# Kernel optimization log

Hardware: AMD Instinct MI355X
Metric: run time of the kernel (lower is better)

The kernel has to match this reference:

```python
import jax, jax.numpy as jnp
import numpy as np

DIM = 1536
N_HEADS = 12
HEAD_DIM = DIM // N_HEADS  # 128
EPS = 1e-6
B, L = 2, 2048


def _rms_norm(x, g, eps=EPS):
    # WanRMSNorm: normalize in fp32 over last dim, scale by g
    xf = x.astype(jnp.float32)
    y = xf * jax.lax.rsqrt(jnp.mean(xf * xf, axis=-1, keepdims=True) + eps)
    return (y * g).astype(x.dtype)


def _apply_rotary(x, freqs):
    # x: [b, s, n, d]; freqs: [1, s, 2d] -> cos/sin each [1, s, 1, d]
    cos, sin = jnp.split(freqs[:, :, None, :], 2, axis=-1)
    b, s, n, d = x.shape
    xr = x.reshape(b, s, n, d // 2, 2)
    rot = jnp.stack([-xr[..., 1], xr[..., 0]], axis=-1).reshape(b, s, n, d)
    out = x.astype(jnp.float32) * cos + rot.astype(jnp.float32) * sin
    return out.astype(x.dtype)


def setup_inputs() -> dict:
    key = jax.random.key(0)
    ks = jax.random.split(key, 12)
    scale = 1.0 / np.sqrt(DIM)
    x = jax.random.normal(ks[0], (B, L, DIM), dtype=jnp.float32)
    wq = jax.random.normal(ks[1], (DIM, DIM), dtype=jnp.float32) * scale
    bq = jnp.zeros((DIM,), dtype=jnp.float32)
    wk = jax.random.normal(ks[2], (DIM, DIM), dtype=jnp.float32) * scale
    bk = jnp.zeros((DIM,), dtype=jnp.float32)
    wv = jax.random.normal(ks[3], (DIM, DIM), dtype=jnp.float32) * scale
    bv = jnp.zeros((DIM,), dtype=jnp.float32)
    wo = jax.random.normal(ks[4], (DIM, DIM), dtype=jnp.float32) * scale
    bo = jnp.zeros((DIM,), dtype=jnp.float32)
    gq = jnp.ones((DIM,), dtype=jnp.float32)
    gk = jnp.ones((DIM,), dtype=jnp.float32)
    # real RoPE table: interleaved-pair cos/sin, concatenated -> [1, L, 2*HEAD_DIM]
    half = HEAD_DIM // 2
    inv_freq = 1.0 / (10000.0 ** (np.arange(half, dtype=np.float32) / half))
    ang = np.arange(L, dtype=np.float32)[:, None] * inv_freq[None, :]  # [L, half]
    cos = np.repeat(np.cos(ang), 2, axis=-1)  # [L, HEAD_DIM]
    sin = np.repeat(np.sin(ang), 2, axis=-1)
    freqs = jnp.asarray(np.concatenate([cos, sin], axis=-1)[None])  # [1, L, 2*HEAD_DIM]
    seq_lens = jnp.array([L, 3 * L // 4], dtype=jnp.int32)
    grid_sizes = jnp.array([[16, 16, 8], [16, 12, 8]], dtype=jnp.int32)
    return {"x": x, "wq": wq, "bq": bq, "wk": wk, "bk": bk, "wv": wv, "bv": bv,
            "wo": wo, "bo": bo, "gq": gq, "gk": gk, "freqs": freqs,
            "seq_lens": seq_lens, "grid_sizes": grid_sizes}


def reference(x, wq, bq, wk, bk, wv, bv, wo, bo, gq, gk, freqs, seq_lens, grid_sizes):
    b, s, _ = x.shape
    n, d = N_HEADS, HEAD_DIM
    q = _rms_norm(x @ wq.T + bq, gq).reshape(b, s, n, d)
    k = _rms_norm(x @ wk.T + bk, gk).reshape(b, s, n, d)
    v = (x @ wv.T + bv).reshape(b, s, n, d)
    q = _apply_rotary(q, freqs)
    k = _apply_rotary(k, freqs)
    # variable-length attention: mask keys j >= seq_lens[b]; window (-1,-1) = full
    scores = jnp.einsum("bqnd,bknd->bnqk", q, k) * (1.0 / np.sqrt(d))
    key_mask = (jnp.arange(s)[None, :] < seq_lens[:, None])[:, None, None, :]  # [b,1,1,s]
    scores = jnp.where(key_mask, scores, jnp.finfo(scores.dtype).min)
    probs = jax.nn.softmax(scores, axis=-1)
    out = jnp.einsum("bnqk,bknd->bqnd", probs, v).reshape(b, s, n * d)
    return out @ wo.T + bo
```

## Files before the change

### kernel.cpp

```cpp
#include <hip/hip_runtime.h>
#include <stdint.h>

typedef unsigned short u16;
typedef __bf16 bfx8 __attribute__((ext_vector_type(8)));
typedef short  sx4  __attribute__((ext_vector_type(4)));
typedef float  fx4  __attribute__((ext_vector_type(4)));
typedef float  fx16 __attribute__((ext_vector_type(16)));
typedef u16    ux8  __attribute__((ext_vector_type(8)));
typedef u16    ux4  __attribute__((ext_vector_type(4)));
typedef float  flt4 __attribute__((ext_vector_type(4)));

#define DIM   1536
#define NH    12
#define HD    128
#define BATCH 2
#define SEQ   2048
#define MTOK  (BATCH*SEQ)
#define EPSV  1e-6f
#define SCALE 0.08838834764831845f
#define NX    (MTOK*DIM)
#define NW    (DIM*DIM)

__device__ __forceinline__ u16 f2bf(float x){
  union { float f; uint32_t u; } v; v.f = x;
  return (u16)((v.u + 0x7FFFu + ((v.u >> 16) & 1u)) >> 16);
}
__device__ __forceinline__ float bf2f(u16 h){
  union { uint32_t u; float f; } v; v.u = ((uint32_t)h) << 16; return v.f;
}
__device__ __forceinline__ void gl_lds16(const void* g, void* l){
  __builtin_amdgcn_global_load_lds((const __attribute__((address_space(1))) void*)g,
                                   (__attribute__((address_space(3))) void*)l, 16, 0, 0);
}
__device__ __forceinline__ fx4 fzero(){ fx4 z = {0.f,0.f,0.f,0.f}; return z; }

__global__ __launch_bounds__(256)
void convert_k(const float* __restrict__ x, const float* __restrict__ wq,
               const float* __restrict__ wk, const float* __restrict__ wv,
               const float* __restrict__ wo,
               u16* __restrict__ xb, u16* __restrict__ wqb, u16* __restrict__ wkb,
               u16* __restrict__ wvb, u16* __restrict__ wob)
{
  const long i4 = (long)(blockIdx.x * 256 + threadIdx.x) * 4;
  const float* src; u16* dst; long off;
  if (i4 < NX){ src = x; dst = xb; off = i4; }
  else {
    long j = i4 - NX;
    if      (j < (long)NW)   { src = wq; dst = wqb; off = j; }
    else if (j < 2L*NW)      { src = wk; dst = wkb; off = j - NW; }
    else if (j < 3L*NW)      { src = wv; dst = wvb; off = j - 2L*NW; }
    else                     { src = wo; dst = wob; off = j - 3L*NW; }
  }
  flt4 v = *(const flt4*)(src + off);
  ux4 o;
  o[0] = f2bf(v[0]); o[1] = f2bf(v[1]); o[2] = f2bf(v[2]); o[3] = f2bf(v[3]);
  *(ux4*)(dst + off) = o;
}

#define BM 128
#define BN 128
#define BK 64
#define NKIT (DIM/BK)

template<int MODE>
__device__ __forceinline__ void gemm_core(char* smem,
                                          const u16* __restrict__ A, const u16* __restrict__ W,
                                          const float* __restrict__ bias,
                                          u16* __restrict__ outb, float* __restrict__ outf,
                                          float* __restrict__ sumsq, u16* __restrict__ vtout)
{
  const int t = threadIdx.x;
  const int lane = t & 63;
  const int wid = t >> 6;
  const int wm = wid >> 1, wn = wid & 1;
  const int quad = lane >> 4, l15 = lane & 15;

  const int lin = blockIdx.y * 12 + blockIdx.x;
  const int r   = lin >> 3;
  const int m0  = ((lin & 7) + 8 * (r / 12)) * BM;
  const int n0  = (r % 12) * BN;

  fx4 acc[4][4];
  #pragma unroll
  for (int i = 0; i < 4; ++i)
    #pragma unroll
    for (int j = 0; j < 4; ++j) acc[i][j] = fzero();

  const int ri  = t >> 3;
  const int sg0 = t & 7;

  auto stage = [&](int kb, int p){
    const int k0 = kb * BK;
    char* base = smem + p * 32768;
    #pragma unroll
    for (int s = 0; s < 4; ++s){
      const int row = s*32 + ri;
      const int sa = sg0 ^ (row & 7);
      gl_lds16(A + (size_t)(m0+row)*DIM + k0 + sa*8, base + s*4096 + t*16);
      gl_lds16(W + (size_t)(n0+row)*DIM + k0 + sa*8, base + 16384 + s*4096 + t*16);
    }
  };

  stage(0, 0);
  for (int kb = 0; kb < NKIT; ++kb){
    char* cur = smem + (kb & 1) * 32768;
    __syncthreads();
    if (kb + 1 < NKIT) stage(kb + 1, (kb + 1) & 1);
    #pragma unroll
    for (int kk = 0; kk < 2; ++kk){
      bfx8 af[4], bw[4];
      #pragma unroll
      for (int i = 0; i < 4; ++i){
        const int rA = wm*64 + i*16 + l15;
        af[i] = *(const bfx8*)(cur + rA*128 + (((kk*4 + quad) ^ (rA & 7)) * 16));
        const int rB = wn*64 + i*16 + l15;
        bw[i] = *(const bfx8*)(cur + 16384 + rB*128 + (((kk*4 + quad) ^ (rB & 7)) * 16));
      }
      #pragma unroll
      for (int i = 0; i < 4; ++i)
        #pragma unroll
        for (int j = 0; j < 4; ++j)
          acc[i][j] = __builtin_amdgcn_mfma_f32_16x16x32_bf16(af[i], bw[j], acc[i][j], 0, 0, 0);
    }
  }

  float bvals[4];
  #pragma unroll
  for (int j = 0; j < 4; ++j) bvals[j] = bias[n0 + wn*64 + j*16 + l15];

  if (MODE == 1){
    u16* T = (u16*)smem;
    #pragma unroll
    for (int i = 0; i < 4; ++i){
      const int row0  = wm*64 + i*16 + quad*4;
      const int chunk = row0 >> 3;
      const int half  = quad & 1;
      #pragma unroll
      for (int j = 0; j < 4; ++j){
        const int col = wn*64 + j*16 + l15;
        ux4 w4;
        #pragma unroll
        for (int rr = 0; rr < 4; ++rr) w4[rr] = f2bf(acc[i][j][rr] + bvals[j]);
        *(ux4*)((char*)T + col*256 + ((chunk ^ (col & 15)) << 4) + half*8) = w4;
      }
    }
    __syncthreads();
    const int b   = m0 >> 11;
    const int m0l = m0 & (SEQ - 1);
    const int cr  = t & 15;
    #pragma unroll
    for (int s = 0; s < 8; ++s){
      const int cl = s*16 + (t >> 4);
      const ux8 v = *(const ux8*)((char*)T + cl*256 + ((cr ^ (cl & 15)) << 4));
      const int cg = n0 + cl;
      const int hh = cg >> 7, dd = cg & (HD - 1);
      *(ux8*)(vtout + (size_t)((b*NH + hh)*HD + dd)*SEQ + m0l + cr*8) = v;
    }
    return;
  }

  #pragma unroll
  for (int i = 0; i < 4; ++i){
    #pragma unroll
    for (int rr = 0; rr < 4; ++rr){
      const int grow = m0 + wm*64 + i*16 + quad*4 + rr;
      float s2 = 0.f;
      #pragma unroll
      for (int j = 0; j < 4; ++j){
        const int gcol = n0 + wn*64 + j*16 + l15;
        const float v = acc[i][j][rr] + bvals[j];
        if (MODE == 2) outf[(size_t)grow*DIM + gcol] = v;
        else           outb[(size_t)grow*DIM + gcol] = f2bf(v);
        s2 += v*v;
      }
      if (MODE == 0){
        s2 += __shfl_xor(s2, 1);
        s2 += __shfl_xor(s2, 2);
        s2 += __shfl_xor(s2, 4);
        s2 += __shfl_xor(s2, 8);
        if (l15 == 0) atomicAdd(&sumsq[grow], s2);
      }
    }
  }
}

__global__ __launch_bounds__(256)
void gemm_qkv_k(const u16* __restrict__ xb,
                const u16* __restrict__ wqb, const u16* __restrict__ wkb, const u16* __restrict__ wvb,
                const float* __restrict__ bq, const float* __restrict__ bk, const float* __restrict__ bv,
                u16* __restrict__ qraw, u16* __restrict__ kraw, u16* __restrict__ vt,
                float* __restrict__ ssq, float* __restrict__ ssk)
{
  __shared__ char smem[65536];
  const int z = blockIdx.z;
  if (z == 0)      gemm_core<0>(smem, xb, wqb, bq, qraw, nullptr, ssq, nullptr);
  else if (z == 1) gemm_core<0>(smem, xb, wkb, bk, kraw, nullptr, ssk, nullptr);
  else             gemm_core<1>(smem, xb, wvb, bv, nullptr, nullptr, nullptr, vt);
}

__global__ __launch_bounds__(256)
void gemm_out_k(const u16* __restrict__ attnb, const u16* __restrict__ wob,
                const float* __restrict__ bo, float* __restrict__ out)
{
  __shared__ char smem[65536];
  gemm_core<2>(smem, attnb, wob, bo, nullptr, out, nullptr, nullptr);
}

__global__ __launch_bounds__(256)
void normrope_k(const u16* __restrict__ qraw, const u16* __restrict__ kraw,
                const float* __restrict__ ssq, const float* __restrict__ ssk,
                const float* __restrict__ gq, const float* __restrict__ gk,
                const float* __restrict__ freqs,
                u16* __restrict__ qbf, u16* __restrict__ kbf)
{
  const int row = blockIdx.x;
  const int isK = blockIdx.y;
  const u16* src   = isK ? kraw : qraw;
  const float* ss  = isK ? ssk  : ssq;
  const float* g   = isK ? gk   : gq;
  u16* dst         = isK ? kbf  : qbf;
  const int spos = row & (SEQ - 1);
  float rstd = rsqrtf(ss[row] * (1.0f/DIM) + EPSV);
  if (!isK) rstd *= SCALE;
  #pragma unroll
  for (int it = 0; it < 3; ++it){
    const int p = threadIdx.x + it*256;
    const int d = p*2;
    const int hd = d & (HD-1);
    const uint32_t two = *(const uint32_t*)(src + (size_t)row*DIM + d);
    const float y0 = bf2f((u16)(two & 0xFFFFu)) * rstd * g[d];
    const float y1 = bf2f((u16)(two >> 16))     * rstd * g[d+1];
    const float c  = freqs[spos*(2*HD) + hd];
    const float sn = freqs[spos*(2*HD) + HD + hd];
    const float o0 = y0*c - y1*sn;
    const float o1 = y1*c + y0*sn;
    *(uint32_t*)(dst + (size_t)row*DIM + d) = (uint32_t)f2bf(o0) | ((uint32_t)f2bf(o1) << 16);
  }
}

__global__ __launch_bounds__(256, 3)
void flash_k(const u16* __restrict__ qbf, const u16* __restrict__ kbf, const u16* __restrict__ vt,
             const int* __restrict__ seq_lens, u16* __restrict__ attnb)
{
  __shared__ char smem[50176];
  const int t = threadIdx.x;
  const int lane = t & 63;
  const int h = lane >> 5;
  const int l31 = lane & 31;
  const int wq = (t >> 6) & 1;
  const int wk = t >> 7;

  const int u  = blockIdx.x;
  const int qt = (u >> 3) & 31;
  const int pr = (u & 7) + 8 * (u >> 8);
  const int hh = pr % 12;
  const int b  = pr / 12;

  const int q0 = qt * 64 + wq * 32;
  const int tokbase = b * SEQ;
  const int kvlen = min(seq_lens[b], SEQ);
  const int ntiles = (kvlen + 63) >> 6;

  bfx8 qf[8];
  {
    const u16* qp = qbf + (size_t)(tokbase + q0 + l31)*DIM + hh*HD + h*8;
    #pragma unroll
    for (int c = 0; c < 8; ++c) qf[c] = *(const bfx8*)(qp + c*16);
  }

  fx16 o[4];
  #pragma unroll
  for (int dt = 0; dt < 4; ++dt)
    #pragma unroll
    for (int r = 0; r < 16; ++r) o[dt][r] = 0.f;
  float mrow = -1e30f, lrow = 0.f;

  const int kri = t >> 4, kseg = t & 15;
  const int vri = t >> 3, vseg = t & 7;
  const int krow = wk*32 + l31;

  #pragma unroll
  for (int s = 0; s < 4; ++s){
    const int row = s*16 + kri;
    const int sg = kseg ^ (row & 15);
    gl_lds16(kbf + (size_t)(tokbase + row)*DIM + hh*HD + sg*8, smem + s*4096 + t*16);
  }

  for (int kt = 0; kt < ntiles; ++kt){
    char* kbuf = smem + (kt & 1) * 16384;
    __syncthreads();

    {
      #pragma unroll
      for (int s = 0; s < 4; ++s){
        const int row = s*32 + vri;
        const int sg = vseg ^ (row & 7);
        gl_lds16(vt + (size_t)((b*NH + hh)*HD + row)*SEQ + kt*64 + sg*8, smem + 32768 + s*4096 + t*16);
      }
    }
    if (kt + 1 < ntiles){
      char* knext = smem + ((kt + 1) & 1) * 16384;
      #pragma unroll
      for (int s = 0; s < 4; ++s){
        const int row = s*16 + kri;
        const int sg = kseg ^ (row & 15);
        gl_lds16(kbf + (size_t)(tokbase + (kt+1)*64 + row)*DIM + hh*HD + sg*8, knext + s*4096 + t*16);
      }
    }

    fx16 st;
    #pragma unroll
    for (int r = 0; r < 16; ++r) st[r] = 0.f;
    #pragma unroll
    for (int c = 0; c < 8; ++c){
      const bfx8 kf = *(const bfx8*)(kbuf + krow*256 + (((2*c + h) ^ (krow & 15)) << 4));
      st = __builtin_amdgcn_mfma_f32_32x32x16_bf16(kf, qf[c], st, 0, 0, 0);
    }

    if ((kt == ntiles - 1) && (kvlen & 63)){
      #pragma unroll
      for (int r = 0; r < 16; ++r){
        const int key = kt*64 + wk*32 + (r & 3) + 8*(r >> 2) + 4*h;
        if (key >= kvlen) st[r] = -1e30f;
      }
    }

    float tm = st[0];
    #pragma unroll
    for (int r = 1; r < 16; ++r) tm = fmaxf(tm, st[r]);
    tm = fmaxf(tm, __shfl_xor(tm, 32));
    if (__any(tm > mrow)){
      const float mnew = fmaxf(mrow, tm);
      const float alpha = __expf(mrow - mnew);
      lrow *= alpha;
      #pragma unroll
      for (int dt = 0; dt < 4; ++dt)
        #pragma unroll
        for (int r = 0; r < 16; ++r) o[dt][r] *= alpha;
      mrow = mnew;
    }

    uint32_t tt[16];
    float ps = 0.f;
    #pragma unroll
    for (int r = 0; r < 16; ++r){
      union { float f; uint32_t u; } e; e.f = __expf(st[r] - mrow);
      const uint32_t uu = e.u + 0x8000u;
      tt[r] = uu;
      union { uint32_t u; float f; } pm; pm.u = uu & 0xFFFF0000u;
      ps += pm.f;
    }
    ps += __shfl_xor(ps, 32);
    lrow += ps;

    sx4 pb[4];
    #pragma unroll
    for (int ks = 0; ks < 4; ++ks){
      union { uint32_t u[2]; sx4 s; } pk;
      pk.u[0] = __builtin_amdgcn_perm(tt[4*ks+1], tt[4*ks+0], 0x07060302u);
      pk.u[1] = __builtin_amdgcn_perm(tt[4*ks+3], tt[4*ks+2], 0x07060302u);
      pb[ks] = pk.s;
    }

    __syncthreads();

    #pragma unroll
    for (int ks = 0; ks < 4; ++ks){
      #pragma unroll
      for (int dt = 0; dt < 4; ++dt){
        const int row = dt*32 + l31;
        const sx4 vf = *(const sx4*)(smem + 32768 + row*128 + ((((wk<<2) + ks) ^ (row & 7)) << 4) + (h << 3));
        o[dt] = __builtin_amdgcn_mfma_f32_32x32x8bf16_1k(vf, pb[ks], o[dt], 0, 0, 0);
      }
    }
  }

  __syncthreads();
  float* mlbuf = (float*)(smem + 49152);
  if (h == 0){
    mlbuf[((wk*2 + wq)*2 + 0)*32 + l31] = mrow;
    mlbuf[((wk*2 + wq)*2 + 1)*32 + l31] = lrow;
  }
  __syncthreads();
  const float mo = mlbuf[(((wk^1)*2 + wq)*2 + 0)*32 + l31];
  const float lo = mlbuf[(((wk^1)*2 + wq)*2 + 1)*32 + l31];
  const float M  = fmaxf(mrow, mo);
  const float f  = __expf(mrow - M);
  const float L  = lrow * f + lo * __expf(mo - M);
  #pragma unroll
  for (int dt = 0; dt < 4; ++dt)
    #pragma unroll
    for (int r = 0; r < 16; ++r) o[dt][r] *= f;
  __syncthreads();

  char* xbuf = smem;
  const int qrow = wq*32 + l31;
  if (wk == 1){
    #pragma unroll
    for (int dt = 0; dt < 4; ++dt)
      #pragma unroll
      for (int rq = 0; rq < 4; ++rq){
        const int d = dt*32 + 8*rq + 4*h;
        fx4 v4; v4[0]=o[dt][4*rq]; v4[1]=o[dt][4*rq+1]; v4[2]=o[dt][4*rq+2]; v4[3]=o[dt][4*rq+3];
        *(fx4*)(xbuf + qrow*512 + (((d >> 2) ^ (qrow & 31)) << 4)) = v4;
      }
  }
  __syncthreads();

  char* Os = smem + 32768;
  if (wk == 0){
    const float invL = 1.0f / L;
    #pragma unroll
    for (int dt = 0; dt < 4; ++dt)
      #pragma unroll
      for (int rq = 0; rq < 4; ++rq){
        const int d = dt*32 + 8*rq + 4*h;
        const fx4 p4 = *(const fx4*)(xbuf + qrow*512 + (((d >> 2) ^ (qrow & 31)) << 4));
        ux4 b4;
        #pragma unroll
        for (int j = 0; j < 4; ++j) b4[j] = f2bf((o[dt][4*rq + j] + p4[j]) * invL);
        *(ux4*)(Os + qrow*256 + (((d >> 3) ^ (qrow & 15)) << 4) + (d & 4)*2) = b4;
      }
  }
  __syncthreads();
  {
    const int ri = t >> 4, seg = t & 15;
    #pragma unroll
    for (int s = 0; s < 4; ++s){
      const int row = s*16 + ri;
      const ux8 val = *(const ux8*)(Os + row*256 + ((seg ^ (row & 15)) << 4));
      *(ux8*)(attnb + (size_t)(tokbase + qt*64 + row)*DIM + hh*HD + seg*8) = val;
    }
  }
}

extern "C" void kernel_launch(void* const* d_in, const int* in_sizes, int n_in,
                              void* d_out, int out_size, void* d_ws, size_t ws_size,
                              hipStream_t stream)
{
  (void)in_sizes; (void)n_in; (void)out_size; (void)ws_size;
  const float* x      = (const float*)d_in[0];
  const float* wq     = (const float*)d_in[1];
  const float* bq     = (const float*)d_in[2];
  const float* wk     = (const float*)d_in[3];
  const float* bk     = (const float*)d_in[4];
  const float* wv     = (const float*)d_in[5];
  const float* bv     = (const float*)d_in[6];
  const float* wo     = (const float*)d_in[7];
  const float* bo     = (const float*)d_in[8];
  const float* gq     = (const float*)d_in[9];
  const float* gk     = (const float*)d_in[10];
  const float* freqs  = (const float*)d_in[11];
  const int*   seqls  = (const int*)d_in[12];

  char* ws = (char*)d_ws;
  u16* xb   = (u16*)(ws + 0);
  u16* wqb  = (u16*)(ws + 12582912);
  u16* wkb  = (u16*)(ws + 17301504);
  u16* wvb  = (u16*)(ws + 22020096);
  u16* wob  = (u16*)(ws + 26738688);
  u16* qraw = (u16*)(ws + 31457280);
  u16* kraw = (u16*)(ws + 44040192);
  u16* vt   = (u16*)(ws + 56623104);
  u16* qbf  = (u16*)(ws + 69206016);
  u16* kbf  = (u16*)(ws + 81788928);
  float* ssq = (float*)(ws + 94371840);
  float* ssk = (float*)(ws + 94388224);
  u16* attnb = qraw;

  (void)hipMemsetAsync(ssq, 0, 32768, stream);

  convert_k   <<<15360, 256, 0, stream>>>(x, wq, wk, wv, wo, xb, wqb, wkb, wvb, wob);
  gemm_qkv_k  <<<dim3(12, 32, 3), 256, 0, stream>>>(xb, wqb, wkb, wvb, bq, bk, bv,
                                                    qraw, kraw, vt, ssq, ssk);
  normrope_k  <<<dim3(4096, 2), 256, 0, stream>>>(qraw, kraw, ssq, ssk, gq, gk, freqs, qbf, kbf);
  flash_k     <<<dim3(768), 256, 0, stream>>>(qbf, kbf, vt, seqls, attnb);
  gemm_out_k  <<<dim3(12, 32), 256, 0, stream>>>(attnb, wob, bo, (float*)d_out);
}
```

Baseline: 322.0 us.

## Load GEMM B operand directly to registers and use 32x32x16 MFMA in attention PV

The GEMM core stops staging the weight tile through shared memory. Each wave now loads its B fragments straight from global memory into registers, software-pipelined one k-half ahead, which halves LDS usage to 32 KB and may allow higher occupancy. In attention, the P·V product switches from the 32x32x8 MFMA to the 32x32x16 bf16 MFMA, using cross-half lane shuffles to build the 8-element P operands. This risks uncoalesced or redundant global weight reads, since the waves sharing a column tile each fetch the same W rows, and it adds extra shuffle work per tile.

```diff
diff --git a/kernel.cpp b/kernel.cpp
--- a/kernel.cpp
+++ b/kernel.cpp
@@ -89,39 +89,58 @@
   const int ri  = t >> 3;
   const int sg0 = t & 7;
 
-  auto stage = [&](int kb, int p){
+  auto stageA = [&](int kb, int p){
     const int k0 = kb * BK;
-    char* base = smem + p * 32768;
+    char* base = smem + p * 16384;
     #pragma unroll
     for (int s = 0; s < 4; ++s){
       const int row = s*32 + ri;
       const int sa = sg0 ^ (row & 7);
       gl_lds16(A + (size_t)(m0+row)*DIM + k0 + sa*8, base + s*4096 + t*16);
-      gl_lds16(W + (size_t)(n0+row)*DIM + k0 + sa*8, base + 16384 + s*4096 + t*16);
     }
   };
 
-  stage(0, 0);
+  const u16* Wp = W + (size_t)(n0 + wn*64 + l15)*DIM + quad*8;
+  auto loadB = [&](int kb, int kk, bfx8* bw){
+    #pragma unroll
+    for (int j = 0; j < 4; ++j)
+      bw[j] = *(const bfx8*)(Wp + (size_t)j*16*DIM + kb*64 + kk*32);
+  };
+
+  stageA(0, 0);
+  bfx8 bw0[4], bw1[4];
+  loadB(0, 0, bw0);
+
   for (int kb = 0; kb < NKIT; ++kb){
-    char* cur = smem + (kb & 1) * 32768;
+    char* cur = smem + (kb & 1) * 16384;
     __syncthreads();
-    if (kb + 1 < NKIT) stage(kb + 1, (kb + 1) & 1);
-    #pragma unroll
-    for (int kk = 0; kk < 2; ++kk){
-      bfx8 af[4], bw[4];
-      #pragma unroll
-      for (int i = 0; i < 4; ++i){
-        const int rA = wm*64 + i*16 + l15;
-        af[i] = *(const bfx8*)(cur + rA*128 + (((kk*4 + quad) ^ (rA & 7)) * 16));
-        const int rB = wn*64 + i*16 + l15;
-        bw[i] = *(const bfx8*)(cur + 16384 + rB*128 + (((kk*4 + quad) ^ (rB & 7)) * 16));
-      }
-      #pragma unroll
-      for (int i = 0; i < 4; ++i)
-        #pragma unroll
-        for (int j = 0; j < 4; ++j)
-          acc[i][j] = __builtin_amdgcn_mfma_f32_16x16x32_bf16(af[i], bw[j], acc[i][j], 0, 0, 0);
-    }
+    if (kb + 1 < NKIT) stageA(kb + 1, (kb + 1) & 1);
+    loadB(kb, 1, bw1);
+
+    bfx8 af[4];
+    #pragma unroll
+    for (int i = 0; i < 4; ++i){
+      const int rA = wm*64 + i*16 + l15;
+      af[i] = *(const bfx8*)(cur + rA*128 + ((quad ^ (rA & 7)) * 16));
+    }
+    #pragma unroll
+    for (int i = 0; i < 4; ++i)
+      #pragma unroll
+      for (int j = 0; j < 4; ++j)
+        acc[i][j] = __builtin_amdgcn_mfma_f32_16x16x32_bf16(af[i], bw0[j], acc[i][j], 0, 0, 0);
+
+    if (kb + 1 < NKIT) loadB(kb + 1, 0, bw0);
+
+    #pragma unroll
+    for (int i = 0; i < 4; ++i){
+      const int rA = wm*64 + i*16 + l15;
+      af[i] = *(const bfx8*)(cur + rA*128 + (((4 + quad) ^ (rA & 7)) * 16));
+    }
+    #pragma unroll
+    for (int i = 0; i < 4; ++i)
+      #pragma unroll
+      for (int j = 0; j < 4; ++j)
+        acc[i][j] = __builtin_amdgcn_mfma_f32_16x16x32_bf16(af[i], bw1[j], acc[i][j], 0, 0, 0);
   }
 
   float bvals[4];
@@ -129,6 +148,7 @@
   for (int j = 0; j < 4; ++j) bvals[j] = bias[n0 + wn*64 + j*16 + l15];
 
   if (MODE == 1){
+    __syncthreads();
     u16* T = (u16*)smem;
     #pragma unroll
     for (int i = 0; i < 4; ++i){
@@ -191,7 +211,7 @@
                 u16* __restrict__ qraw, u16* __restrict__ kraw, u16* __restrict__ vt,
                 float* __restrict__ ssq, float* __restrict__ ssk)
 {
-  __shared__ char smem[65536];
+  __shared__ char smem[32768];
   const int z = blockIdx.z;
   if (z == 0)      gemm_core<0>(smem, xb, wqb, bq, qraw, nullptr, ssq, nullptr);
   else if (z == 1) gemm_core<0>(smem, xb, wkb, bk, kraw, nullptr, ssk, nullptr);
@@ -202,7 +222,7 @@
 void gemm_out_k(const u16* __restrict__ attnb, const u16* __restrict__ wob,
                 const float* __restrict__ bo, float* __restrict__ out)
 {
-  __shared__ char smem[65536];
+  __shared__ char smem[32768];
   gemm_core<2>(smem, attnb, wob, bo, nullptr, out, nullptr, nullptr);
 }
 
@@ -340,37 +360,47 @@
       mrow = mnew;
     }
 
-    uint32_t tt[16];
+    uint32_t w8[8];
     float ps = 0.f;
     #pragma unroll
-    for (int r = 0; r < 16; ++r){
-      union { float f; uint32_t u; } e; e.f = __expf(st[r] - mrow);
-      const uint32_t uu = e.u + 0x8000u;
-      tt[r] = uu;
-      union { uint32_t u; float f; } pm; pm.u = uu & 0xFFFF0000u;
-      ps += pm.f;
+    for (int j = 0; j < 8; ++j){
+      union { float f; uint32_t u; } e0, e1;
+      e0.f = __expf(st[2*j]   - mrow);
+      e1.f = __expf(st[2*j+1] - mrow);
+      const uint32_t u0 = e0.u + 0x8000u, u1 = e1.u + 0x8000u;
+      w8[j] = __builtin_amdgcn_perm(u1, u0, 0x07060302u);
+      union { uint32_t u; float f; } p0, p1;
+      p0.u = u0 & 0xFFFF0000u; p1.u = u1 & 0xFFFF0000u;
+      ps += p0.f + p1.f;
     }
     ps += __shfl_xor(ps, 32);
     lrow += ps;
 
-    sx4 pb[4];
-    #pragma unroll
-    for (int ks = 0; ks < 4; ++ks){
-      union { uint32_t u[2]; sx4 s; } pk;
-      pk.u[0] = __builtin_amdgcn_perm(tt[4*ks+1], tt[4*ks+0], 0x07060302u);
-      pk.u[1] = __builtin_amdgcn_perm(tt[4*ks+3], tt[4*ks+2], 0x07060302u);
-      pb[ks] = pk.s;
-    }
+    const uint32_t s0 = h ? w8[0] : w8[2];
+    const uint32_t s1 = h ? w8[1] : w8[3];
+    const uint32_t s2 = h ? w8[4] : w8[6];
+    const uint32_t s3 = h ? w8[5] : w8[7];
+    const uint32_t r0 = (uint32_t)__shfl_xor((int)s0, 32);
+    const uint32_t r1 = (uint32_t)__shfl_xor((int)s1, 32);
+    const uint32_t r2 = (uint32_t)__shfl_xor((int)s2, 32);
+    const uint32_t r3 = (uint32_t)__shfl_xor((int)s3, 32);
+    union { uint32_t u[4]; bfx8 v; } pb0, pb1;
+    pb0.u[0] = h ? r0 : w8[0]; pb0.u[1] = h ? r1 : w8[1];
+    pb0.u[2] = h ? w8[2] : r0; pb0.u[3] = h ? w8[3] : r1;
+    pb1.u[0] = h ? r2 : w8[4]; pb1.u[1] = h ? r3 : w8[5];
+    pb1.u[2] = h ? w8[6] : r2; pb1.u[3] = h ? w8[7] : r3;
 
     __syncthreads();
 
     #pragma unroll
-    for (int ks = 0; ks < 4; ++ks){
+    for (int km = 0; km < 2; ++km){
+      const bfx8 pB = km ? pb1.v : pb0.v;
       #pragma unroll
       for (int dt = 0; dt < 4; ++dt){
         const int row = dt*32 + l31;
-        const sx4 vf = *(const sx4*)(smem + 32768 + row*128 + ((((wk<<2) + ks) ^ (row & 7)) << 4) + (h << 3));
-        o[dt] = __builtin_amdgcn_mfma_f32_32x32x8bf16_1k(vf, pb[ks], o[dt], 0, 0, 0);
+        const int c = (wk << 2) + 2*km + h;
+        const bfx8 vf = *(const bfx8*)(smem + 32768 + row*128 + ((c ^ (row & 7)) << 4));
+        o[dt] = __builtin_amdgcn_mfma_f32_32x32x16_bf16(vf, pB, o[dt], 0, 0, 0);
       }
     }
   }
```

After: 408.5 us. 1.27x slower.
